# Performance work log

Measured on AMD Instinct MI355X. Metric: run time of the kernel, lower is better.

Reference implementation:

```python
import jax, jax.numpy as jnp
import numpy as np

QMAX = 127.0  # symmetric int8 fake quantization

def fake_quant(t):
    # per-tensor symmetric int8 fake quant: scale = max|t|/127
    scale = jnp.max(jnp.abs(t)) / QMAX
    scale = jnp.maximum(scale, 1e-8)
    q = jnp.clip(jnp.round(t / scale), -QMAX, QMAX)
    return q * scale

def setup_inputs() -> dict:
    key = jax.random.key(0)
    k1, k2, k3 = jax.random.split(key, 3)
    B, S, D_IN, D_OUT = 8, 2048, 4096, 4096
    x = jax.random.normal(k1, (B, S, D_IN), dtype=jnp.float32)
    # kaiming_uniform-like init scale
    bound = np.sqrt(6.0 / D_IN)
    weights = jax.random.uniform(k2, (D_OUT, D_IN), dtype=jnp.float32, minval=-bound, maxval=bound)
    stdv = 1.0 / np.sqrt(D_IN)
    bias = jax.random.uniform(k3, (D_OUT,), dtype=jnp.float32, minval=-stdv, maxval=stdv)
    return {"x": x, "weights": weights, "bias": bias}

def reference(x, weights, bias):
    x_q = fake_quant(x)          # quantize activations
    w_q = fake_quant(weights)    # quantize weights
    # F.linear: x @ W^T + b
    return jnp.einsum('bsi,oi->bso', x_q, w_q) + bias
```

## Files before the change

kernel.cpp:

```cpp
#include <hip/hip_runtime.h>
#include <cstddef>
#include <cstdint>


typedef int i32x4 __attribute__((ext_vector_type(4)));

__device__ __forceinline__ void async16(const void* g, void* l) {
    __builtin_amdgcn_global_load_lds(
        (const __attribute__((address_space(1))) void*)g,
        (__attribute__((address_space(3))) void*)l,
        16, 0, 0);
}

__global__ void absmax_kernel(const float* __restrict__ in, unsigned int n4,
                              unsigned int* __restrict__ out_bits) {
    const float4* in4 = (const float4*)in;
    float m = 0.0f;
    for (unsigned int i = blockIdx.x * blockDim.x + threadIdx.x; i < n4;
         i += gridDim.x * blockDim.x) {
        float4 v = in4[i];
        m = fmaxf(m, fmaxf(fmaxf(fabsf(v.x), fabsf(v.y)),
                           fmaxf(fabsf(v.z), fabsf(v.w))));
    }
    #pragma unroll
    for (int o = 32; o > 0; o >>= 1)
        m = fmaxf(m, __shfl_xor(m, o));
    __shared__ float wmax[8];
    int lane = threadIdx.x & 63;
    int wv = threadIdx.x >> 6;
    if (lane == 0) wmax[wv] = m;
    __syncthreads();
    if (threadIdx.x == 0) {
        int nw = blockDim.x >> 6;
        float b = wmax[0];
        for (int i = 1; i < nw; ++i) b = fmaxf(b, wmax[i]);
        atomicMax(out_bits, __float_as_uint(b));
    }
}

__device__ __forceinline__ int quant4(float4 v, float s) {
    int a = (int)fminf(fmaxf(rintf(v.x / s), -127.0f), 127.0f);
    int b = (int)fminf(fmaxf(rintf(v.y / s), -127.0f), 127.0f);
    int c = (int)fminf(fmaxf(rintf(v.z / s), -127.0f), 127.0f);
    int d = (int)fminf(fmaxf(rintf(v.w / s), -127.0f), 127.0f);
    return (a & 255) | ((b & 255) << 8) | ((c & 255) << 16) | (d << 24);
}

__global__ void quant_kernel(const float* __restrict__ in, char* __restrict__ out,
                             unsigned int n16,
                             const unsigned int* __restrict__ absmax_bits) {
    float s = fmaxf(__uint_as_float(*absmax_bits) / 127.0f, 1e-8f);
    const float4* in4 = (const float4*)in;
    i32x4* out16 = (i32x4*)out;
    for (unsigned int i = blockIdx.x * blockDim.x + threadIdx.x; i < n16;
         i += gridDim.x * blockDim.x) {
        float4 v0 = in4[i * 4 + 0];
        float4 v1 = in4[i * 4 + 1];
        float4 v2 = in4[i * 4 + 2];
        float4 v3 = in4[i * 4 + 3];
        i32x4 q;
        q[0] = quant4(v0, s);
        q[1] = quant4(v1, s);
        q[2] = quant4(v2, s);
        q[3] = quant4(v3, s);
        out16[i] = q;
    }
}

#define BM 256
#define BN 256

__global__ __launch_bounds__(512, 2) void gemm_i8_kernel(
    const char* __restrict__ Aq, const char* __restrict__ Bq,
    const float* __restrict__ bias, float* __restrict__ C,
    const unsigned int* __restrict__ scale_bits, int M, int N, int K) {
    __shared__ char lds[4 * 16384 * 2];
    char* const sA = lds;
    char* const sB = lds + 4 * 16384;

    const int t = threadIdx.x;
    const int lane = t & 63;
    const int w = t >> 6;
    const int wm = w >> 2;
    const int wn = w & 3;

    const int m0 = blockIdx.y * BM;
    const int n0 = blockIdx.x * BN;

    const int sr = t >> 2;
    const int scl = (t & 3) ^ ((t >> 3) & 3);
    const char* gA0 = Aq + (size_t)(m0 + sr) * K + scl * 16;
    const char* gA1 = Aq + (size_t)(m0 + sr + 128) * K + scl * 16;
    const char* gB0 = Bq + (size_t)(n0 + sr) * K + scl * 16;
    const char* gB1 = Bq + (size_t)(n0 + sr + 128) * K + scl * 16;

#define STAGE_A(kt) do { char* d_ = sA + ((kt) & 3) * 16384 + t * 16;          \
        size_t ko_ = (size_t)(kt) * 64;                                        \
        async16(gA0 + ko_, d_); async16(gA1 + ko_, d_ + 8192); } while (0)
#define STAGE_B(kt) do { char* d_ = sB + ((kt) & 3) * 16384 + t * 16;          \
        size_t ko_ = (size_t)(kt) * 64;                                        \
        async16(gB0 + ko_, d_); async16(gB1 + ko_, d_ + 8192); } while (0)

    const int rl = lane & 15;
    const int cg = lane >> 4;
    const int csw = (cg ^ ((rl >> 1) & 3)) << 4;
    const int aoff = wm * 8192 + rl * 64 + csw;
    const int boff = wn * 4096 + rl * 64 + csw;

    i32x4 acc[8][4] = {};

    const int NT = K >> 6;

    STAGE_A(0); STAGE_B(0);
    STAGE_A(1); STAGE_B(1);
    STAGE_A(2); STAGE_B(2);
    asm volatile("s_waitcnt vmcnt(8)" ::: "memory");
    __builtin_amdgcn_s_barrier();

#define MFMA_ROW(ai, AF)                                                        \
    acc[ai][0] = __builtin_amdgcn_mfma_i32_16x16x64_i8(AF, bf0, acc[ai][0], 0, 0, 0); \
    acc[ai][1] = __builtin_amdgcn_mfma_i32_16x16x64_i8(AF, bf1, acc[ai][1], 0, 0, 0); \
    acc[ai][2] = __builtin_amdgcn_mfma_i32_16x16x64_i8(AF, bf2, acc[ai][2], 0, 0, 0); \
    acc[ai][3] = __builtin_amdgcn_mfma_i32_16x16x64_i8(AF, bf3, acc[ai][3], 0, 0, 0);

    for (int kt = 0; kt < NT; ++kt) {
        const char* cA = sA + (kt & 3) * 16384;
        const char* cB = sB + (kt & 3) * 16384;

        i32x4 af0 = *(const i32x4*)(cA + aoff);
        i32x4 af1 = *(const i32x4*)(cA + aoff + 1024);
        i32x4 af2 = *(const i32x4*)(cA + aoff + 2048);
        i32x4 af3 = *(const i32x4*)(cA + aoff + 3072);
        i32x4 bf0 = *(const i32x4*)(cB + boff);
        i32x4 bf1 = *(const i32x4*)(cB + boff + 1024);
        i32x4 bf2 = *(const i32x4*)(cB + boff + 2048);
        i32x4 bf3 = *(const i32x4*)(cB + boff + 3072);
        if (kt + 3 < NT) STAGE_A(kt + 3);
        __builtin_amdgcn_s_barrier();
        asm volatile("s_waitcnt lgkmcnt(0)" ::: "memory");
        __builtin_amdgcn_sched_barrier(0);
        __builtin_amdgcn_s_setprio(1);
        MFMA_ROW(0, af0)
        MFMA_ROW(1, af1)
        MFMA_ROW(2, af2)
        MFMA_ROW(3, af3)
        __builtin_amdgcn_s_setprio(0);
        __builtin_amdgcn_s_barrier();

        af0 = *(const i32x4*)(cA + aoff + 4096);
        af1 = *(const i32x4*)(cA + aoff + 5120);
        af2 = *(const i32x4*)(cA + aoff + 6144);
        af3 = *(const i32x4*)(cA + aoff + 7168);
        if (kt + 3 < NT) STAGE_B(kt + 3);
        __builtin_amdgcn_s_barrier();
        asm volatile("s_waitcnt lgkmcnt(0)" ::: "memory");
        __builtin_amdgcn_sched_barrier(0);
        __builtin_amdgcn_s_setprio(1);
        MFMA_ROW(4, af0)
        MFMA_ROW(5, af1)
        MFMA_ROW(6, af2)
        MFMA_ROW(7, af3)
        __builtin_amdgcn_s_setprio(0);
        if (kt < NT - 3) {
            asm volatile("s_waitcnt vmcnt(8)" ::: "memory");
        } else if (kt == NT - 3) {
            asm volatile("s_waitcnt vmcnt(4)" ::: "memory");
        } else if (kt == NT - 2) {
            asm volatile("s_waitcnt vmcnt(0)" ::: "memory");
        }
        __builtin_amdgcn_s_barrier();
    }

    float sx = fmaxf(__uint_as_float(scale_bits[0]) / 127.0f, 1e-8f);
    float sw = fmaxf(__uint_as_float(scale_bits[1]) / 127.0f, 1e-8f);
    float s = sx * sw;

    const int crow = m0 + wm * 128 + cg * 4;
    const int ccol = n0 + wn * 64 + rl;
    #pragma unroll
    for (int nt = 0; nt < 4; ++nt) {
        int col = ccol + nt * 16;
        float bv = bias[col];
        #pragma unroll
        for (int mt = 0; mt < 8; ++mt) {
            float* Cp = C + (size_t)(crow + mt * 16) * N + col;
            #pragma unroll
            for (int r = 0; r < 4; ++r)
                Cp[(size_t)r * N] = (float)acc[mt][nt][r] * s + bv;
        }
    }
}

extern "C" void kernel_launch(void* const* d_in, const int* in_sizes, int n_in,
                              void* d_out, int out_size, void* d_ws, size_t ws_size,
                              hipStream_t stream) {
    const float* x = (const float*)d_in[0];
    const float* w = (const float*)d_in[1];
    const float* bias = (const float*)d_in[2];
    float* out = (float*)d_out;

    const int N = in_sizes[2];
    const int K = in_sizes[1] / N;
    const int M = in_sizes[0] / K;

    unsigned int* scale_bits = (unsigned int*)d_ws;
    char* xq = (char*)d_ws + 256;
    char* wq = xq + (size_t)M * K;

    const unsigned int nx4 = (unsigned int)((size_t)M * K / 4);
    const unsigned int nw4 = (unsigned int)((size_t)N * K / 4);
    const unsigned int nx16 = nx4 / 4;
    const unsigned int nw16 = nw4 / 4;

    hipMemsetAsync(d_ws, 0, 16, stream);

    absmax_kernel<<<2048, 256, 0, stream>>>(x, nx4, scale_bits + 0);
    absmax_kernel<<<1024, 256, 0, stream>>>(w, nw4, scale_bits + 1);

    quant_kernel<<<2048, 256, 0, stream>>>(x, xq, nx16, scale_bits + 0);
    quant_kernel<<<1024, 256, 0, stream>>>(w, wq, nw16, scale_bits + 1);

    dim3 grid(N / BN, M / BM);
    gemm_i8_kernel<<<grid, 512, 0, stream>>>(xq, wq, bias, out, scale_bits, M, N, K);
}
```

Baseline: 828.7 us.

## Switch GEMM to 32x32x32 MFMA with register double-buffered fragments and fused prep kernels

The GEMM moves from 16x16x64 to 32x32x32 int8 MFMA, prefetching the next k-tile's A/B fragments into registers across two unrolled half-iterations. This removes the mid-iteration barriers and lgkmcnt waits of the old loop. It also remaps workgroups with an XCD-aware block swizzle for L2 locality, and merges the separate absmax and quant kernels for x and w into single launches. The quant kernel now uses nontemporal loads. In exchange, register pressure rises and the hand-tuned vmcnt accounting becomes harder to keep correct.

```diff
diff --git a/kernel.cpp b/kernel.cpp
--- a/kernel.cpp
+++ b/kernel.cpp
@@ -4,6 +4,8 @@
 
 
 typedef int i32x4 __attribute__((ext_vector_type(4)));
+typedef int i32x16 __attribute__((ext_vector_type(16)));
+typedef float f32x4 __attribute__((ext_vector_type(4)));
 
 __device__ __forceinline__ void async16(const void* g, void* l) {
     __builtin_amdgcn_global_load_lds(
@@ -12,12 +14,17 @@
         16, 0, 0);
 }
 
-__global__ void absmax_kernel(const float* __restrict__ in, unsigned int n4,
-                              unsigned int* __restrict__ out_bits) {
-    const float4* in4 = (const float4*)in;
+__global__ void absmax2_kernel(const float* __restrict__ x, unsigned int nx4,
+                               const float* __restrict__ w, unsigned int nw4,
+                               unsigned int* __restrict__ out_bits) {
+    const bool isW = (blockIdx.x >= 2048);
+    const float4* in4 = (const float4*)(isW ? w : x);
+    const unsigned int n4 = isW ? nw4 : nx4;
+    const unsigned int stride = (isW ? 512u : 2048u) * blockDim.x;
+    const unsigned int start =
+        (isW ? (blockIdx.x - 2048) : blockIdx.x) * blockDim.x + threadIdx.x;
     float m = 0.0f;
-    for (unsigned int i = blockIdx.x * blockDim.x + threadIdx.x; i < n4;
-         i += gridDim.x * blockDim.x) {
+    for (unsigned int i = start; i < n4; i += stride) {
         float4 v = in4[i];
         m = fmaxf(m, fmaxf(fmaxf(fabsf(v.x), fabsf(v.y)),
                            fmaxf(fabsf(v.z), fabsf(v.w))));
@@ -25,7 +32,7 @@
     #pragma unroll
     for (int o = 32; o > 0; o >>= 1)
         m = fmaxf(m, __shfl_xor(m, o));
-    __shared__ float wmax[8];
+    __shared__ float wmax[4];
     int lane = threadIdx.x & 63;
     int wv = threadIdx.x >> 6;
     if (lane == 0) wmax[wv] = m;
@@ -34,30 +41,35 @@
         int nw = blockDim.x >> 6;
         float b = wmax[0];
         for (int i = 1; i < nw; ++i) b = fmaxf(b, wmax[i]);
-        atomicMax(out_bits, __float_as_uint(b));
-    }
-}
-
-__device__ __forceinline__ int quant4(float4 v, float s) {
-    int a = (int)fminf(fmaxf(rintf(v.x / s), -127.0f), 127.0f);
-    int b = (int)fminf(fmaxf(rintf(v.y / s), -127.0f), 127.0f);
-    int c = (int)fminf(fmaxf(rintf(v.z / s), -127.0f), 127.0f);
-    int d = (int)fminf(fmaxf(rintf(v.w / s), -127.0f), 127.0f);
+        atomicMax(out_bits + (isW ? 1 : 0), __float_as_uint(b));
+    }
+}
+
+__device__ __forceinline__ int quant4(f32x4 v, float s) {
+    int a = (int)fminf(fmaxf(rintf(v[0] / s), -127.0f), 127.0f);
+    int b = (int)fminf(fmaxf(rintf(v[1] / s), -127.0f), 127.0f);
+    int c = (int)fminf(fmaxf(rintf(v[2] / s), -127.0f), 127.0f);
+    int d = (int)fminf(fmaxf(rintf(v[3] / s), -127.0f), 127.0f);
     return (a & 255) | ((b & 255) << 8) | ((c & 255) << 16) | (d << 24);
 }
 
-__global__ void quant_kernel(const float* __restrict__ in, char* __restrict__ out,
-                             unsigned int n16,
-                             const unsigned int* __restrict__ absmax_bits) {
-    float s = fmaxf(__uint_as_float(*absmax_bits) / 127.0f, 1e-8f);
-    const float4* in4 = (const float4*)in;
-    i32x4* out16 = (i32x4*)out;
-    for (unsigned int i = blockIdx.x * blockDim.x + threadIdx.x; i < n16;
-         i += gridDim.x * blockDim.x) {
-        float4 v0 = in4[i * 4 + 0];
-        float4 v1 = in4[i * 4 + 1];
-        float4 v2 = in4[i * 4 + 2];
-        float4 v3 = in4[i * 4 + 3];
+__global__ void quant2_kernel(const float* __restrict__ x, char* __restrict__ xq,
+                              unsigned int nx16, const float* __restrict__ w,
+                              char* __restrict__ wq, unsigned int nw16,
+                              const unsigned int* __restrict__ scale_bits) {
+    const bool isW = (blockIdx.x >= 2048);
+    const f32x4* in4 = (const f32x4*)(isW ? w : x);
+    i32x4* out16 = (i32x4*)(isW ? wq : xq);
+    const unsigned int n16 = isW ? nw16 : nx16;
+    const unsigned int stride = (isW ? 512u : 2048u) * blockDim.x;
+    const unsigned int start =
+        (isW ? (blockIdx.x - 2048) : blockIdx.x) * blockDim.x + threadIdx.x;
+    float s = fmaxf(__uint_as_float(scale_bits[isW ? 1 : 0]) / 127.0f, 1e-8f);
+    for (unsigned int i = start; i < n16; i += stride) {
+        f32x4 v0 = __builtin_nontemporal_load(in4 + i * 4 + 0);
+        f32x4 v1 = __builtin_nontemporal_load(in4 + i * 4 + 1);
+        f32x4 v2 = __builtin_nontemporal_load(in4 + i * 4 + 2);
+        f32x4 v3 = __builtin_nontemporal_load(in4 + i * 4 + 3);
         i32x4 q;
         q[0] = quant4(v0, s);
         q[1] = quant4(v1, s);
@@ -84,8 +96,12 @@
     const int wm = w >> 2;
     const int wn = w & 3;
 
-    const int m0 = blockIdx.y * BM;
-    const int n0 = blockIdx.x * BN;
+    const int nwgx = gridDim.x;
+    const int id = blockIdx.y * nwgx + blockIdx.x;
+    const int cpx = (nwgx * gridDim.y) >> 3;
+    const int swzid = (id & 7) * cpx + (id >> 3);
+    const int m0 = (swzid / nwgx) * BM;
+    const int n0 = (swzid % nwgx) * BN;
 
     const int sr = t >> 2;
     const int scl = (t & 3) ^ ((t >> 3) & 3);
@@ -101,92 +117,102 @@
         size_t ko_ = (size_t)(kt) * 64;                                        \
         async16(gB0 + ko_, d_); async16(gB1 + ko_, d_ + 8192); } while (0)
 
-    const int rl = lane & 15;
-    const int cg = lane >> 4;
-    const int csw = (cg ^ ((rl >> 1) & 3)) << 4;
-    const int aoff = wm * 8192 + rl * 64 + csw;
-    const int boff = wn * 4096 + rl * 64 + csw;
-
-    i32x4 acc[8][4] = {};
+    const int rl32 = lane & 31;
+    const int kh = lane >> 5;
+    const int swz0 = ((kh ^ ((rl32 >> 1) & 3)) << 4);
+    const int swz1 = (((2 + kh) ^ ((rl32 >> 1) & 3)) << 4);
+    const int arow = wm * 8192 + rl32 * 64;
+    const int brow = wn * 4096 + rl32 * 64;
+
+#define RD_A(slot, mt, s) (*(const i32x4*)((slot) + arow + (mt) * 2048 + ((s) ? swz1 : swz0)))
+#define RD_B(slot, j, s)  (*(const i32x4*)((slot) + brow + (j) * 2048 + ((s) ? swz1 : swz0)))
+
+    i32x16 acc[4][2] = {};
+    i32x4 a00, a01, a10, a11;
+    i32x4 a20, a21, a30, a31;
+    i32x4 p00, p01, p10, p11;
+    i32x4 q00, q01, q10, q11;
 
     const int NT = K >> 6;
+
+#define MM(acc_, a_, b_) acc_ = __builtin_amdgcn_mfma_i32_32x32x32_i8(a_, b_, acc_, 0, 0, 0)
+
+#define PH1(cA_, kt3_, B00, B01, B10, B11)                                     \
+    a20 = RD_A(cA_, 2, 0); a21 = RD_A(cA_, 2, 1);                              \
+    a30 = RD_A(cA_, 3, 0); a31 = RD_A(cA_, 3, 1);                              \
+    if ((kt3_) < NT) STAGE_A(kt3_);                                            \
+    __builtin_amdgcn_sched_barrier(0);                                         \
+    __builtin_amdgcn_s_setprio(1);                                             \
+    MM(acc[0][0], a00, B00); MM(acc[0][1], a00, B10);                          \
+    MM(acc[1][0], a10, B00); MM(acc[1][1], a10, B10);                          \
+    MM(acc[0][0], a01, B01); MM(acc[0][1], a01, B11);                          \
+    MM(acc[1][0], a11, B01); MM(acc[1][1], a11, B11);                          \
+    __builtin_amdgcn_s_setprio(0);
+
+#define PH2(cAn_, cBn_, kt3_, doRead_, B00, B01, B10, B11, N00, N01, N10, N11) \
+    if (doRead_) {                                                             \
+        a00 = RD_A(cAn_, 0, 0); a01 = RD_A(cAn_, 0, 1);                        \
+        a10 = RD_A(cAn_, 1, 0); a11 = RD_A(cAn_, 1, 1);                        \
+        N00 = RD_B(cBn_, 0, 0); N01 = RD_B(cBn_, 0, 1);                        \
+        N10 = RD_B(cBn_, 1, 0); N11 = RD_B(cBn_, 1, 1);                        \
+    }                                                                          \
+    if ((kt3_) < NT) STAGE_B(kt3_);                                            \
+    __builtin_amdgcn_sched_barrier(0);                                         \
+    __builtin_amdgcn_s_setprio(1);                                             \
+    MM(acc[2][0], a20, B00); MM(acc[2][1], a20, B10);                          \
+    MM(acc[3][0], a30, B00); MM(acc[3][1], a30, B10);                          \
+    MM(acc[2][0], a21, B01); MM(acc[2][1], a21, B11);                          \
+    MM(acc[3][0], a31, B01); MM(acc[3][1], a31, B11);                          \
+    __builtin_amdgcn_s_setprio(0);
+
+#define TILE_END(kt_)                                                          \
+    if ((kt_) + 3 < NT) { asm volatile("s_waitcnt vmcnt(4)" ::: "memory"); }   \
+    else                { asm volatile("s_waitcnt vmcnt(0)" ::: "memory"); }   \
+    __builtin_amdgcn_s_barrier();
 
     STAGE_A(0); STAGE_B(0);
     STAGE_A(1); STAGE_B(1);
     STAGE_A(2); STAGE_B(2);
-    asm volatile("s_waitcnt vmcnt(8)" ::: "memory");
+    asm volatile("s_waitcnt vmcnt(4)" ::: "memory");
     __builtin_amdgcn_s_barrier();
-
-#define MFMA_ROW(ai, AF)                                                        \
-    acc[ai][0] = __builtin_amdgcn_mfma_i32_16x16x64_i8(AF, bf0, acc[ai][0], 0, 0, 0); \
-    acc[ai][1] = __builtin_amdgcn_mfma_i32_16x16x64_i8(AF, bf1, acc[ai][1], 0, 0, 0); \
-    acc[ai][2] = __builtin_amdgcn_mfma_i32_16x16x64_i8(AF, bf2, acc[ai][2], 0, 0, 0); \
-    acc[ai][3] = __builtin_amdgcn_mfma_i32_16x16x64_i8(AF, bf3, acc[ai][3], 0, 0, 0);
-
-    for (int kt = 0; kt < NT; ++kt) {
-        const char* cA = sA + (kt & 3) * 16384;
-        const char* cB = sB + (kt & 3) * 16384;
-
-        i32x4 af0 = *(const i32x4*)(cA + aoff);
-        i32x4 af1 = *(const i32x4*)(cA + aoff + 1024);
-        i32x4 af2 = *(const i32x4*)(cA + aoff + 2048);
-        i32x4 af3 = *(const i32x4*)(cA + aoff + 3072);
-        i32x4 bf0 = *(const i32x4*)(cB + boff);
-        i32x4 bf1 = *(const i32x4*)(cB + boff + 1024);
-        i32x4 bf2 = *(const i32x4*)(cB + boff + 2048);
-        i32x4 bf3 = *(const i32x4*)(cB + boff + 3072);
-        if (kt + 3 < NT) STAGE_A(kt + 3);
-        __builtin_amdgcn_s_barrier();
-        asm volatile("s_waitcnt lgkmcnt(0)" ::: "memory");
-        __builtin_amdgcn_sched_barrier(0);
-        __builtin_amdgcn_s_setprio(1);
-        MFMA_ROW(0, af0)
-        MFMA_ROW(1, af1)
-        MFMA_ROW(2, af2)
-        MFMA_ROW(3, af3)
-        __builtin_amdgcn_s_setprio(0);
-        __builtin_amdgcn_s_barrier();
-
-        af0 = *(const i32x4*)(cA + aoff + 4096);
-        af1 = *(const i32x4*)(cA + aoff + 5120);
-        af2 = *(const i32x4*)(cA + aoff + 6144);
-        af3 = *(const i32x4*)(cA + aoff + 7168);
-        if (kt + 3 < NT) STAGE_B(kt + 3);
-        __builtin_amdgcn_s_barrier();
-        asm volatile("s_waitcnt lgkmcnt(0)" ::: "memory");
-        __builtin_amdgcn_sched_barrier(0);
-        __builtin_amdgcn_s_setprio(1);
-        MFMA_ROW(4, af0)
-        MFMA_ROW(5, af1)
-        MFMA_ROW(6, af2)
-        MFMA_ROW(7, af3)
-        __builtin_amdgcn_s_setprio(0);
-        if (kt < NT - 3) {
-            asm volatile("s_waitcnt vmcnt(8)" ::: "memory");
-        } else if (kt == NT - 3) {
-            asm volatile("s_waitcnt vmcnt(4)" ::: "memory");
-        } else if (kt == NT - 2) {
-            asm volatile("s_waitcnt vmcnt(0)" ::: "memory");
-        }
-        __builtin_amdgcn_s_barrier();
+    a00 = RD_A(sA, 0, 0); a01 = RD_A(sA, 0, 1);
+    a10 = RD_A(sA, 1, 0); a11 = RD_A(sA, 1, 1);
+    p00 = RD_B(sB, 0, 0); p01 = RD_B(sB, 0, 1);
+    p10 = RD_B(sB, 1, 0); p11 = RD_B(sB, 1, 1);
+
+    for (int kt = 0; kt < NT; kt += 2) {
+        const char* cA0 = sA + ((kt) & 3) * 16384;
+        const char* cA1 = sA + ((kt + 1) & 3) * 16384;
+        const char* cB1 = sB + ((kt + 1) & 3) * 16384;
+        const char* cA2 = sA + ((kt + 2) & 3) * 16384;
+        const char* cB2 = sB + ((kt + 2) & 3) * 16384;
+
+        PH1(cA0, kt + 3, p00, p01, p10, p11)
+        PH2(cA1, cB1, kt + 3, 1, p00, p01, p10, p11, q00, q01, q10, q11)
+        TILE_END(kt)
+
+        PH1(cA1, kt + 4, q00, q01, q10, q11)
+        PH2(cA2, cB2, kt + 4, (kt + 2 < NT), q00, q01, q10, q11, p00, p01, p10, p11)
+        TILE_END(kt + 1)
     }
 
     float sx = fmaxf(__uint_as_float(scale_bits[0]) / 127.0f, 1e-8f);
     float sw = fmaxf(__uint_as_float(scale_bits[1]) / 127.0f, 1e-8f);
     float s = sx * sw;
 
-    const int crow = m0 + wm * 128 + cg * 4;
-    const int ccol = n0 + wn * 64 + rl;
+    const int rbase = m0 + wm * 128 + 4 * kh;
+    const int cbase = n0 + wn * 64 + rl32;
     #pragma unroll
-    for (int nt = 0; nt < 4; ++nt) {
-        int col = ccol + nt * 16;
-        float bv = bias[col];
+    for (int mt = 0; mt < 4; ++mt) {
         #pragma unroll
-        for (int mt = 0; mt < 8; ++mt) {
-            float* Cp = C + (size_t)(crow + mt * 16) * N + col;
+        for (int j = 0; j < 2; ++j) {
+            int col = cbase + j * 32;
+            float bv = bias[col];
             #pragma unroll
-            for (int r = 0; r < 4; ++r)
-                Cp[(size_t)r * N] = (float)acc[mt][nt][r] * s + bv;
+            for (int r = 0; r < 16; ++r) {
+                int row = rbase + mt * 32 + (r & 3) + 8 * (r >> 2);
+                C[(size_t)row * N + col] = (float)acc[mt][j][r] * s + bv;
+            }
         }
     }
 }
@@ -209,16 +235,11 @@
 
     const unsigned int nx4 = (unsigned int)((size_t)M * K / 4);
     const unsigned int nw4 = (unsigned int)((size_t)N * K / 4);
-    const unsigned int nx16 = nx4 / 4;
-    const unsigned int nw16 = nw4 / 4;
 
     hipMemsetAsync(d_ws, 0, 16, stream);
 
-    absmax_kernel<<<2048, 256, 0, stream>>>(x, nx4, scale_bits + 0);
-    absmax_kernel<<<1024, 256, 0, stream>>>(w, nw4, scale_bits + 1);
-
-    quant_kernel<<<2048, 256, 0, stream>>>(x, xq, nx16, scale_bits + 0);
-    quant_kernel<<<1024, 256, 0, stream>>>(w, wq, nw16, scale_bits + 1);
+    absmax2_kernel<<<2560, 256, 0, stream>>>(x, nx4, w, nw4, scale_bits);
+    quant2_kernel<<<2560, 256, 0, stream>>>(x, xq, nx4 / 4, w, wq, nw4 / 4, scale_bits);
 
     dim3 grid(N / BN, M / BM);
     gemm_i8_kernel<<<grid, 512, 0, stream>>>(xq, wq, bias, out, scale_bits, M, N, K);
```

Result: faster. 807.6 us (-2.5%).
